# Kernel tuning notes

Hardware: AMD Instinct MI355X
Metric: run time of the kernel (lower is better)

## Reference

```python
import jax, jax.numpy as jnp
import numpy as np

DIM = 512
K_ALL = 11
K_TOP = 4
DOMAIN = 10
EPS = 1e-12
NEG_INF = -1e30

def _normalize(x):
    n = jnp.linalg.norm(x, axis=-1, keepdims=True)
    return x / jnp.maximum(n, EPS)

def _leaky(x):
    return jax.nn.leaky_relu(x, 0.01)

def setup_inputs():
    key = jax.random.key(0)
    ks = jax.random.split(key, 16)
    Bp, Lp, Bg, Lg = 128, 256, 64, 512
    probes = jax.random.normal(ks[0], (1, Bp, Lp, DIM), jnp.float32)
    gallery = jax.random.normal(ks[1], (1, Bg, Lg, DIM), jnp.float32)
    probe_lengths = jax.random.randint(ks[2], (1, Bp), 1, Lp + 1)
    gallery_lengths = jax.random.randint(ks[3], (1, Bg), 1, Lg + 1)
    proxies_p = jax.random.normal(ks[4], (K_ALL, DIM), jnp.float32) * 0.06
    proxies_g = jax.random.normal(ks[5], (K_ALL, DIM), jnp.float32) * 0.06
    transform_W = jax.random.normal(ks[6], (DOMAIN, DIM), jnp.float32) * 0.06
    transform_b = jnp.zeros((DOMAIN,), jnp.float32)
    probe_W = jnp.eye(DIM, dtype=jnp.float32)  # nn.init.eye_
    probe_b = jnp.zeros((DIM,), jnp.float32)
    # pooler MLP weights stacked over the 11 experts; init_weights: N(0, 0.001), zero bias
    pool_W1 = jax.random.normal(ks[7], (K_ALL, 2 * DIM, 3 * DIM), jnp.float32) * 1e-3
    pool_b1 = jnp.zeros((K_ALL, 2 * DIM), jnp.float32)
    pool_W2 = jax.random.normal(ks[8], (K_ALL, 2 * DIM, 2 * DIM), jnp.float32) * 1e-3
    pool_b2 = jnp.zeros((K_ALL, 2 * DIM), jnp.float32)
    pool_W3 = jax.random.normal(ks[9], (K_ALL, DIM, 2 * DIM), jnp.float32) * 1e-3
    pool_b3 = jnp.zeros((K_ALL, DIM), jnp.float32)
    return dict(probes=probes, gallery=gallery, probe_lengths=probe_lengths,
                gallery_lengths=gallery_lengths, proxies_p=proxies_p, proxies_g=proxies_g,
                transform_W=transform_W, transform_b=transform_b, probe_W=probe_W,
                probe_b=probe_b, pool_W1=pool_W1, pool_b1=pool_b1, pool_W2=pool_W2,
                pool_b2=pool_b2, pool_W3=pool_W3, pool_b3=pool_b3)

def reference(probes, gallery, probe_lengths, gallery_lengths, proxies_p, proxies_g,
              transform_W, transform_b, probe_W, probe_b,
              pool_W1, pool_b1, pool_W2, pool_b2, pool_W3, pool_b3):
    def fuse(feat, length, proxies, use_probe_linear):
        # feat: [L, D], length: scalar int; masked equivalent of feat[:length]
        L = feat.shape[0]
        fmask = (jnp.arange(L) < length).astype(feat.dtype)[:, None]  # [L, 1]
        lp = jnp.maximum(length, 1).astype(feat.dtype)
        normed = _normalize(feat)
        tf = _normalize(feat @ transform_W.T + transform_b)        # [L, 10]
        tp = _normalize(proxies @ transform_W.T + transform_b)      # [K_ALL, 10]
        sims = tf @ tp.T                                            # [L, K_ALL]
        gsim = (sims * fmask).sum(0)                                # [K_ALL]
        _, idx = jax.lax.top_k(gsim, K_TOP)
        mean = (feat * fmask).sum(0) / lp                           # [D]
        var = (((feat - mean) ** 2) * fmask).sum(0) / lp            # biased variance
        summary = jnp.concatenate([jnp.tile(mean[None], (K_TOP, 1)),
                                   jnp.tile(var[None], (K_TOP, 1)),
                                   proxies[idx]], axis=-1)          # [K_TOP, 3D]
        # expert-gathered pooler MLPs (dropout = identity in eval)
        h = _leaky(jnp.einsum('koi,ki->ko', pool_W1[idx], summary) + pool_b1[idx])
        h = _leaky(jnp.einsum('koi,ki->ko', pool_W2[idx], h) + pool_b2[idx])
        ctx = _leaky(jnp.einsum('koi,ki->ko', pool_W3[idx], h) + pool_b3[idx])  # [K_TOP, D]
        q = feat @ probe_W.T + probe_b if use_probe_linear else feat
        scores = q @ ctx.T                                          # [L, K_TOP]
        scores = jnp.where(fmask > 0, scores, NEG_INF)
        w = jax.nn.softmax(scores, axis=0)                          # softmax over set dim
        return jnp.einsum('ld,lk->kd', normed, w)                   # [K_TOP, D]

    p, g = probes[0], gallery[0]
    pl, gl = probe_lengths[0], gallery_lengths[0]
    final_probe = jax.vmap(lambda f, l: fuse(f, l, proxies_p, True))(p, pl)
    final_gallery = jax.vmap(lambda f, l: fuse(f, l, proxies_g, False))(g, gl)
    return (final_probe,
            proxies_p @ transform_W.T + transform_b,
            final_gallery,
            proxies_g @ transform_W.T + transform_b)
```

## Files before the change

### kernel.cpp

```cpp
#include <hip/hip_runtime.h>
#include <hip/hip_bf16.h>

namespace {

using us = unsigned short;
typedef __attribute__((ext_vector_type(8))) short bf16x8;
typedef __attribute__((ext_vector_type(4))) float f32x4;
typedef __attribute__((ext_vector_type(4))) unsigned short us4;
typedef __attribute__((ext_vector_type(4))) unsigned int u32x4;

constexpr int DIM_ = 512, KALL = 11, DOM = 10, NPROBE = 128, NSETS = 192;
constexpr int LPR = 256, LGA = 512;

constexpr size_t O_OUT1 = 0;
constexpr size_t O_OUT2 = (size_t)NPROBE * 4 * DIM_;
constexpr size_t O_OUT3 = O_OUT2 + KALL * DOM;
constexpr size_t O_OUT4 = O_OUT3 + (size_t)64 * 4 * DIM_;

constexpr size_t F_TP   = 64;
constexpr size_t F_IDX  = 320;
constexpr size_t F_S0A  = 1600;
constexpr size_t F_WQ   = 4096;
constexpr size_t F_GP   = 495616;
constexpr size_t F_SUMM = 514048;
constexpr size_t F_H1   = 612352;
constexpr size_t F_PART = F_H1;
constexpr size_t F_CTXW = F_H1;
constexpr size_t F_H2   = 1693696;
constexpr size_t F_ACC  = F_H2;
constexpr size_t F_CTX  = 2775040;
constexpr size_t F_WT   = 3315712;
constexpr size_t F_BEFF = 3446784;
constexpr size_t WS_FLOATS = F_BEFF + 2 * KALL * 1024;
constexpr size_t WS_BYTES  = WS_FLOATS * 4;

__device__ __forceinline__ float b2f(us u) { return __uint_as_float(((unsigned)u) << 16); }
__device__ __forceinline__ us f2b(float x) {
    unsigned u = __float_as_uint(x);
    u += 0x7FFF + ((u >> 16) & 1);
    return (us)(u >> 16);
}
__device__ __forceinline__ float ldT(const float* p) { return *p; }
__device__ __forceinline__ float ldT(const us* p) { return b2f(*p); }
__device__ __forceinline__ void stT(float* p, float v) { *p = v; }
__device__ __forceinline__ void stT(us* p, float v) { *p = f2b(v); }

__device__ __forceinline__ bf16x8 loadA(const us* p) { return *(const bf16x8*)p; }
__device__ __forceinline__ bf16x8 loadA(const float* p) {
    f32x4 a = *(const f32x4*)p, b = *(const f32x4*)(p + 4);
    bf16x8 r;
#pragma unroll
    for (int j = 0; j < 4; ++j) { r[j] = (short)f2b(a[j]); r[4 + j] = (short)f2b(b[j]); }
    return r;
}
__device__ __forceinline__ bf16x8 pack8(f32x4 a, f32x4 b) {
    bf16x8 r;
#pragma unroll
    for (int j = 0; j < 4; ++j) { r[j] = (short)f2b(a[j]); r[4 + j] = (short)f2b(b[j]); }
    return r;
}

__device__ __forceinline__ void gload_lds16(const us* g, us* l) {
    __builtin_amdgcn_global_load_lds(
        (const __attribute__((address_space(1))) void*)g,
        (__attribute__((address_space(3))) void*)l, 16, 0, 0);
}

__device__ __forceinline__ void decode64(int bx, int& set, int& base, int& L) {
    if (bx < 512) { set = bx >> 2; base = (bx & 3) * 64; L = LPR; }
    else { set = NPROBE + ((bx - 512) >> 3); base = ((bx - 512) & 7) * 64; L = LGA; }
}

__global__ void detect_kernel(const unsigned int* probeW_bits, int* flag) {
    if (threadIdx.x == 0) *flag = (probeW_bits[0] == 0x3F800000u) ? 0 : 1;
}

template <typename T>
__device__ void proxies_body(const T* pp, const T* pg, const T* tW, const T* tb,
                             float* wsf, T* dout) {
    int b = blockIdx.x;
    int fam = b / KALL, i = b % KALL;
    int lane = threadIdx.x;
    const T* src = fam ? pg : pp;
    float t[DOM];
#pragma unroll
    for (int r = 0; r < DOM; ++r) t[r] = 0.f;
    for (int d = lane; d < DIM_; d += 64) {
        float x = ldT(src + (size_t)i * DIM_ + d);
#pragma unroll
        for (int r = 0; r < DOM; ++r) t[r] += x * ldT(tW + (size_t)r * DIM_ + d);
    }
#pragma unroll
    for (int off = 32; off >= 1; off >>= 1)
#pragma unroll
        for (int r = 0; r < DOM; ++r) t[r] += __shfl_xor(t[r], off, 64);
#pragma unroll
    for (int r = 0; r < DOM; ++r) t[r] += ldT(tb + r);
    float nn = 0.f;
#pragma unroll
    for (int r = 0; r < DOM; ++r) nn += t[r] * t[r];
    float inv = 1.0f / fmaxf(sqrtf(nn), 1e-12f);
    if (lane < DOM) {
        size_t base = fam ? O_OUT4 : O_OUT2;
        stT(dout + base + i * DOM + lane, t[lane]);
        wsf[F_TP + fam * 128 + i * DOM + lane] = t[lane] * inv;
    }
}
__global__ void proxies_kernel(const int* flag, const void* pp, const void* pg,
                               const void* tW, const void* tb, float* wsf, void* dout) {
    if (*flag)
        proxies_body<us>((const us*)pp, (const us*)pg, (const us*)tW, (const us*)tb, wsf, (us*)dout);
    else
        proxies_body<float>((const float*)pp, (const float*)pg, (const float*)tW, (const float*)tb, wsf, (float*)dout);
}

template <typename T>
__device__ void pbias_body(const T* W1, const T* b1, const T* pp, const T* pg, float* beff) {
    int bx = blockIdx.x;
    int e = bx >> 4, ch = bx & 15;
    int tid = threadIdx.x;
    int om = tid >> 2, sub = tid & 3;
    int m = ch * 64 + om;
    const T* wr = W1 + ((size_t)e * 1024 + m) * 1536 + 1024 + sub * 128;
    const T* pr = pp + (size_t)e * DIM_ + sub * 128;
    const T* gr = pg + (size_t)e * DIM_ + sub * 128;
    float sp = 0.f, sg = 0.f;
    if constexpr (sizeof(T) == 2) {
#pragma unroll 4
        for (int k = 0; k < 128; k += 2) {
            unsigned wv = *(const unsigned*)(wr + k);
            unsigned pv = *(const unsigned*)(pr + k);
            unsigned gv = *(const unsigned*)(gr + k);
            float w0 = __uint_as_float(wv << 16), w1 = __uint_as_float(wv & 0xFFFF0000u);
            float p0 = __uint_as_float(pv << 16), p1 = __uint_as_float(pv & 0xFFFF0000u);
            float g0 = __uint_as_float(gv << 16), g1 = __uint_as_float(gv & 0xFFFF0000u);
            sp += w0 * p0 + w1 * p1;
            sg += w0 * g0 + w1 * g1;
        }
    } else {
#pragma unroll 2
        for (int k = 0; k < 128; k += 4) {
            f32x4 wv = *(const f32x4*)(wr + k);
            f32x4 pv = *(const f32x4*)(pr + k);
            f32x4 gv = *(const f32x4*)(gr + k);
#pragma unroll
            for (int q = 0; q < 4; ++q) { sp += wv[q] * pv[q]; sg += wv[q] * gv[q]; }
        }
    }
    sp += __shfl_xor(sp, 1, 64); sp += __shfl_xor(sp, 2, 64);
    sg += __shfl_xor(sg, 1, 64); sg += __shfl_xor(sg, 2, 64);
    if (sub == 0) {
        float bb = ldT(b1 + (size_t)e * 1024 + m);
        beff[(size_t)e * 1024 + m] = bb + sp;
        beff[(size_t)(KALL + e) * 1024 + m] = bb + sg;
    }
}
__global__ void pbias_kernel(const int* flag, const void* W1, const void* b1,
                             const void* pp, const void* pg, float* beff) {
    if (*flag)
        pbias_body<us>((const us*)W1, (const us*)b1, (const us*)pp, (const us*)pg, beff);
    else
        pbias_body<float>((const float*)W1, (const float*)b1, (const float*)pp, (const float*)pg, beff);
}

template <typename T>
__device__ void sims_body(const T* probes, const T* gallery, const int* plen,
                          const int* glen, const T* tW, float* wsf) {
    int bx = blockIdx.x, set, base, L;
    decode64(bx, set, base, L);
    bool probe = set < NPROBE;
    int len = probe ? plen[set] : glen[set - NPROBE];
    int len_eff = min(max(len, 1), L);
    float* GP = wsf + F_GP + (size_t)bx * 12;
    float* PART = wsf + F_PART + (size_t)bx * 1024;
    int tid = threadIdx.x;
    int nvalid = len_eff - base;
    if (nvalid <= 0) {
        if (tid < KALL) GP[tid] = 0.f;
        for (int d = tid; d < 1024; d += 256) PART[d] = 0.f;
        return;
    }
    nvalid = min(nvalid, 64);
    const T* feat = probe ? probes + (size_t)set * L * DIM_
                          : gallery + (size_t)(set - NPROBE) * L * DIM_;
    __shared__ __align__(16) float tile[4][320];
    __shared__ float tpl[KALL * DOM];
    __shared__ float gs[16];
    __shared__ float psum[DIM_], psq[DIM_];
    if (tid < KALL * DOM) tpl[tid] = wsf[F_TP + (probe ? 0 : 128) + tid];
    if (tid < 16) gs[tid] = 0.f;
    psum[tid] = 0.f; psum[tid + 256] = 0.f;
    psq[tid] = 0.f; psq[tid + 256] = 0.f;
    __syncthreads();

    int w = tid >> 6, lane = tid & 63, lm = lane & 15, quad = lane >> 4;

    {
        int cl = lane;
        const T* fb = feat + (size_t)base * DIM_ + cl * 8;
        float asum[8] = {0,0,0,0,0,0,0,0}, asq[8] = {0,0,0,0,0,0,0,0};
        for (int r = w; r < nvalid; r += 8) {
            bool two = (r + 4 < nvalid);
            float f0[8], f1[8];
            if constexpr (sizeof(T) == 2) {
                u32x4 ra = *(const u32x4*)(fb + (size_t)r * DIM_);
                u32x4 rb = two ? *(const u32x4*)(fb + (size_t)(r + 4) * DIM_)
                               : (u32x4){0, 0, 0, 0};
#pragma unroll
                for (int q = 0; q < 4; ++q) {
                    f0[2*q]   = __uint_as_float(ra[q] << 16);
                    f0[2*q+1] = __uint_as_float(ra[q] & 0xFFFF0000u);
                    f1[2*q]   = __uint_as_float(rb[q] << 16);
                    f1[2*q+1] = __uint_as_float(rb[q] & 0xFFFF0000u);
                }
            } else {
                const T* rp = fb + (size_t)r * DIM_;
                f32x4 a0 = *(const f32x4*)rp, a1 = *(const f32x4*)(rp + 4);
#pragma unroll
                for (int j = 0; j < 4; ++j) { f0[j] = a0[j]; f0[4+j] = a1[j]; }
                if (two) {
                    const T* rq = fb + (size_t)(r + 4) * DIM_;
                    f32x4 b0 = *(const f32x4*)rq, b1 = *(const f32x4*)(rq + 4);
#pragma unroll
                    for (int j = 0; j < 4; ++j) { f1[j] = b0[j]; f1[4+j] = b1[j]; }
                } else {
#pragma unroll
                    for (int j = 0; j < 8; ++j) f1[j] = 0.f;
                }
            }
#pragma unroll
            for (int j = 0; j < 8; ++j) {
                asum[j] += f0[j] + f1[j];
                asq[j] += f0[j] * f0[j] + f1[j] * f1[j];
            }
        }
#pragma unroll
        for (int j = 0; j < 8; ++j) {
            atomicAdd(&psum[cl * 8 + j], asum[j]);
            atomicAdd(&psq[cl * 8 + j], asq[j]);
        }
    }
    __syncthreads();
    PART[tid] = psum[tid]; PART[tid + 256] = psum[tid + 256];
    PART[512 + tid] = psq[tid]; PART[768 + tid] = psq[tid + 256];

    bf16x8 bq[16];
#pragma unroll
    for (int s = 0; s < 16; ++s) {
        if (lm < DOM) bq[s] = loadA(tW + (size_t)lm * DIM_ + s * 32 + quad * 8);
        else bq[s] = (bf16x8){0, 0, 0, 0, 0, 0, 0, 0};
    }
    int m0 = base + w * 16;
    const T* Ap = feat + (size_t)(m0 + lm) * DIM_ + quad * 8;
    f32x4 acc = (f32x4){0.f, 0.f, 0.f, 0.f};
    float vsq = 0.f;
#pragma unroll
    for (int s = 0; s < 16; ++s) {
        bf16x8 a;
        if constexpr (sizeof(T) == 2) {
            a = *(const bf16x8*)(Ap + s * 32);
#pragma unroll
            for (int j = 0; j < 8; ++j) { float x = b2f((us)a[j]); vsq += x * x; }
        } else {
            f32x4 p0 = *(const f32x4*)(Ap + s * 32), p1 = *(const f32x4*)(Ap + s * 32 + 4);
#pragma unroll
            for (int j = 0; j < 4; ++j) {
                vsq += p0[j] * p0[j] + p1[j] * p1[j];
                a[j] = (short)f2b(p0[j]); a[4 + j] = (short)f2b(p1[j]);
            }
        }
        acc = __builtin_amdgcn_mfma_f32_16x16x32_bf16(a, bq[s], acc, 0, 0, 0);
    }
    vsq += __shfl_xor(vsq, 16, 64);
    vsq += __shfl_xor(vsq, 32, 64);
    {
        int rown = m0 + lm;
        if (quad == 0 && rown < len_eff)
            wsf[F_WQ + (size_t)set * 2560 + (size_t)rown * 5 + 4] =
                1.0f / fmaxf(sqrtf(vsq), 1e-12f);
    }
#pragma unroll
    for (int r = 0; r < 4; ++r) tile[w][(quad * 4 + r) * 20 + lm] = acc[r];
    __syncthreads();

    float gacc[KALL];
#pragma unroll
    for (int k = 0; k < KALL; ++k) gacc[k] = 0.f;
    if (lane < 16) {
        int row = m0 + lane;
        if (row < len_eff) {
            const float* tr = &tile[w][lane * 20];
            f32x4 t0 = *(const f32x4*)tr, t1 = *(const f32x4*)(tr + 4);
            float tv[DOM] = {t0[0], t0[1], t0[2], t0[3], t1[0], t1[1], t1[2], t1[3], tr[8], tr[9]};
            float nn = 0.f;
#pragma unroll
            for (int r = 0; r < DOM; ++r) nn += tv[r] * tv[r];
            float inv = 1.0f / fmaxf(sqrtf(nn), 1e-12f);
#pragma unroll
            for (int k = 0; k < KALL; ++k) {
                float s = 0.f;
#pragma unroll
                for (int r = 0; r < DOM; ++r) s += tv[r] * tpl[k * DOM + r];
                gacc[k] = s * inv;
            }
        }
    }
#pragma unroll
    for (int off = 8; off >= 1; off >>= 1)
#pragma unroll
        for (int k = 0; k < KALL; ++k) gacc[k] += __shfl_xor(gacc[k], off, 64);
    if (lane == 0)
#pragma unroll
        for (int k = 0; k < KALL; ++k) atomicAdd(&gs[k], gacc[k]);
    __syncthreads();
    if (tid < KALL) GP[tid] = gs[tid];
}
__global__ __launch_bounds__(256, 3) void sims_kernel(const int* flag, const void* probes,
        const void* gallery, const int* plen, const int* glen, const void* tW, float* wsf) {
    if (*flag) sims_body<us>((const us*)probes, (const us*)gallery, plen, glen, (const us*)tW, wsf);
    else sims_body<float>((const float*)probes, (const float*)gallery, plen, glen, (const float*)tW, wsf);
}

__global__ void statsfin_kernel(const int* plen, const int* glen, float* wsf) {
    int set = blockIdx.x, tid = threadIdx.x;
    bool probe = set < NPROBE;
    int len = probe ? plen[set] : glen[set - NPROBE];
    float lp = (float)max(len, 1);
    int nch = probe ? 4 : 8;
    int cb = probe ? set * 4 : 512 + (set - NPROBE) * 8;
    const float* P = wsf + F_PART + (size_t)cb * 1024;
    us* SUMM = (us*)(wsf + F_SUMM);
    for (int d = tid; d < DIM_; d += 256) {
        float s = 0.f, q = 0.f;
        for (int c = 0; c < nch; ++c) {
            s += P[(size_t)c * 1024 + d];
            q += P[(size_t)c * 1024 + 512 + d];
        }
        float m = s / lp;
        float v = q / lp - m * m;
        SUMM[(size_t)set * 1024 + d] = f2b(m);
        SUMM[(size_t)set * 1024 + DIM_ + d] = f2b(v);
    }
    if (tid == 0) {
        int gb = probe ? set * 4 : 512 + (set - NPROBE) * 8;
        float g[KALL];
        for (int i = 0; i < KALL; ++i) {
            float s = 0.f;
            for (int c = 0; c < nch; ++c) s += wsf[F_GP + (size_t)(gb + c) * 12 + i];
            g[i] = s;
        }
        int* idx4 = (int*)(wsf + F_IDX);
        for (int kk = 0; kk < 4; ++kk) {
            int bi = 0; float bv = g[0];
            for (int i = 1; i < KALL; ++i)
                if (g[i] > bv) { bv = g[i]; bi = i; }
            idx4[set * 4 + kk] = bi;
            g[bi] = -3e38f;
        }
    }
}

template <typename T>
__device__ void wt_body(const T* W, us* WT) {
    __shared__ us t[64][65];
    int bi = blockIdx.y * 64, bj = blockIdx.x * 64, tid = threadIdx.x;
    for (int i = tid; i < 4096; i += 256) {
        int r = i >> 6, cc = i & 63;
        t[r][cc] = (sizeof(T) == 2) ? ((const us*)W)[(size_t)(bi + r) * DIM_ + bj + cc]
                                    : f2b(ldT(W + (size_t)(bi + r) * DIM_ + bj + cc));
    }
    __syncthreads();
    for (int i = tid; i < 4096; i += 256) {
        int r = i >> 6, cc = i & 63;
        WT[(size_t)(bj + r) * DIM_ + bi + cc] = t[cc][r];
    }
}
__global__ void wt_kernel(const int* flag, const void* W, us* WT) {
    if (*flag) wt_body<us>((const us*)W, WT);
    else wt_body<float>((const float*)W, WT);
}

template <int M, int KS, int L1>
__global__ __launch_bounds__(256) void mlp_one(const int* flag, const void* Wv,
        const void* biasv, const us* X, us* Y, const float* beff) {
    constexpr int MT = M / 64;
    constexpr int NK = 16;
    int flagv = *flag;
    __shared__ us SM[8192];
    int bx = blockIdx.x;
    int nt = bx / (MT * KALL);
    int rem = bx - nt * (MT * KALL);
    int e = rem % KALL;
    int mt = rem / KALL;
    int tid = threadIdx.x, w = tid >> 6, lane = tid & 63;
    int lm = lane & 15, quad = lane >> 4;
    int s0 = nt * 64;
    const size_t aoff = ((size_t)e * M + mt * 64 + w * 16 + lm) * KS + quad * 8;
    const float* AF = (const float*)Wv + aoff;
    const us*    AB = (const us*)Wv + aoff;
    int xrow0 = (L1 ? 0 : e * NSETS) + s0;
    int slot0 = w * 64 + lane, slot1 = slot0 + 256;
    int brow0 = slot0 >> 3, bcol0 = (slot0 & 7) ^ (brow0 & 7);
    int brow1 = slot1 >> 3, bcol1 = (slot1 & 7) ^ (brow1 & 7);
    const us* Xs0 = X + ((size_t)(xrow0 + brow0)) * 1024 + bcol0 * 8;
    const us* Xs1 = X + ((size_t)(xrow0 + brow1)) * 1024 + bcol1 * 8;
    us* ls0 = SM + slot0 * 8;
    us* ls1 = SM + slot1 * 8;

    f32x4 acc[4];
#pragma unroll
    for (int j = 0; j < 4; ++j) acc[j] = (f32x4){0.f, 0.f, 0.f, 0.f};

    bf16x8 a0[2], a1[2];
    f32x4 pan[4];

    auto issueB = [&](int par, int k0) {
        gload_lds16(Xs0 + k0, ls0 + par * 4096);
        gload_lds16(Xs1 + k0, ls1 + par * 4096);
    };
    auto loadAx = [&](int k0, bf16x8* adst) {
        if (flagv) {
            adst[0] = *(const bf16x8*)(AB + k0);
            adst[1] = *(const bf16x8*)(AB + k0 + 32);
        } else {
            pan[0] = *(const f32x4*)(AF + k0);
            pan[1] = *(const f32x4*)(AF + k0 + 4);
            pan[2] = *(const f32x4*)(AF + k0 + 32);
            pan[3] = *(const f32x4*)(AF + k0 + 36);
        }
    };
    auto packA = [&](bf16x8* adst) {
        if (!flagv) {
            adst[0] = pack8(pan[0], pan[1]);
            adst[1] = pack8(pan[2], pan[3]);
        }
    };
    auto compute = [&](int par, const bf16x8* a) {
        const us* Bb = SM + par * 4096;
#pragma unroll
        for (int ks = 0; ks < 2; ++ks)
#pragma unroll
            for (int j = 0; j < 4; ++j) {
                int br = j * 16 + lm;
                int cg = ks * 4 + quad;
                bf16x8 b = *(const bf16x8*)(Bb + br * 64 + ((cg ^ (br & 7)) * 8));
                acc[j] = __builtin_amdgcn_mfma_f32_16x16x32_bf16(a[ks], b, acc[j], 0, 0, 0);
            }
    };

    issueB(0, 0);
    loadAx(0, a0);
    packA(a0);
    __syncthreads();
#pragma unroll 1
    for (int t = 0; t < NK; t += 2) {
        int k1 = (t + 1) * 64, k2 = (t + 2) * 64;
        if (t + 1 < NK) { issueB(1, k1); loadAx(k1, a1); }
        compute(0, a0);
        if (t + 1 < NK) packA(a1);
        __syncthreads();
        if (t + 1 < NK) {
            if (t + 2 < NK) { issueB(0, k2); loadAx(k2, a0); }
            compute(1, a1);
            if (t + 2 < NK) packA(a0);
            __syncthreads();
        }
    }

    int m0 = mt * 64 + w * 16 + quad * 4;
    float bv[4];
    if (L1) {
        const float* be = beff + ((size_t)((nt < 2) ? 0 : KALL) + e) * 1024 + m0;
#pragma unroll
        for (int r = 0; r < 4; ++r) bv[r] = be[r];
    } else {
#pragma unroll
        for (int r = 0; r < 4; ++r)
            bv[r] = flagv ? b2f(((const us*)biasv)[(size_t)e * M + m0 + r])
                          : ((const float*)biasv)[(size_t)e * M + m0 + r];
    }
#pragma unroll
    for (int j = 0; j < 4; ++j) {
        int s = s0 + j * 16 + lm;
        us4 pk;
#pragma unroll
        for (int r = 0; r < 4; ++r) {
            float v = acc[j][r] + bv[r];
            v = v > 0.f ? v : 0.01f * v;
            pk[r] = f2b(v);
        }
        *(us4*)(Y + ((size_t)e * NSETS + s) * M + m0) = pk;
    }
}

__global__ void fold_kernel(const us* CTX, const us* WT, us* CTXW) {
    int nt = blockIdx.x, mtb = blockIdx.y;
    int e = mtb >> 1, sub = mtb & 1;
    int row0 = e * NSETS + sub * 64;
    int tid = threadIdx.x, w = tid >> 6, lane = tid & 63;
    int lm = lane & 15, quad = lane >> 4, kq = quad * 8;
    const us* Ap = CTX + ((size_t)row0 + w * 16 + lm) * DIM_ + kq;
    int n0 = nt * 64;
    const us* Bp = WT + (size_t)(n0 + lm) * DIM_ + kq;
    f32x4 acc[4];
#pragma unroll
    for (int j = 0; j < 4; ++j) acc[j] = (f32x4){0.f, 0.f, 0.f, 0.f};
#pragma unroll 2
    for (int kc = 0; kc < DIM_; kc += 32) {
        bf16x8 a = *(const bf16x8*)(Ap + kc);
#pragma unroll
        for (int j = 0; j < 4; ++j) {
            bf16x8 b = *(const bf16x8*)(Bp + kc + (size_t)j * 16 * DIM_);
            acc[j] = __builtin_amdgcn_mfma_f32_16x16x32_bf16(a, b, acc[j], 0, 0, 0);
        }
    }
    int mrow = row0 + w * 16 + quad * 4;
#pragma unroll
    for (int j = 0; j < 4; ++j)
#pragma unroll
        for (int r = 0; r < 4; ++r)
            CTXW[(size_t)(mrow + r) * DIM_ + n0 + j * 16 + lm] = f2b(acc[j][r]);
}

template <typename T>
__device__ void s0a_body(const us* CTX, const T* pb, float* S0A) {
    int tid = threadIdx.x, w = tid >> 6, lane = tid & 63;
    int row = blockIdx.x * 4 + w;
    bf16x8 cv = *(const bf16x8*)(CTX + (size_t)row * DIM_ + lane * 8);
    float s = 0.f;
#pragma unroll
    for (int j = 0; j < 8; ++j) s += b2f((us)cv[j]) * ldT(pb + lane * 8 + j);
#pragma unroll
    for (int off = 32; off >= 1; off >>= 1) s += __shfl_xor(s, off, 64);
    if (lane == 0) S0A[row] = s;
}
__global__ void s0a_kernel(const int* flag, const us* CTX, const void* pb, float* S0A) {
    if (*flag) s0a_body<us>(CTX, (const us*)pb, S0A);
    else s0a_body<float>(CTX, (const float*)pb, S0A);
}

template <typename T>
__device__ void score_body(const T* probes, const T* gallery, const int* plen,
                           const int* glen, float* wsf) {
    int bx = blockIdx.x, set, base, L;
    decode64(bx, set, base, L);
    bool probe = set < NPROBE;
    int len = probe ? plen[set] : glen[set - NPROBE];
    int len_eff = min(max(len, 1), L);
    if (base >= len_eff) return;
    const T* feat = probe ? probes + (size_t)set * L * DIM_
                          : gallery + (size_t)(set - NPROBE) * L * DIM_;
    int tid = threadIdx.x, w = tid >> 6, lane = tid & 63;
    int lm = lane & 15, quad = lane >> 4;
    const int* idx4 = (const int*)(wsf + F_IDX);
    const us* CTXW = (const us*)(wsf + F_CTXW);
    const us* CTXR = (const us*)(wsf + F_CTX);
    bf16x8 bq[16];
    float s0v = 0.f;
    if (lm < 4) {
        int row = idx4[set * 4 + lm] * NSETS + set;
        const us* src = (probe ? CTXW : CTXR) + (size_t)row * DIM_ + quad * 8;
#pragma unroll
        for (int s = 0; s < 16; ++s) bq[s] = *(const bf16x8*)(src + s * 32);
        s0v = probe ? wsf[F_S0A + row] : 0.f;
    } else {
#pragma unroll
        for (int s = 0; s < 16; ++s) bq[s] = (bf16x8){0, 0, 0, 0, 0, 0, 0, 0};
    }
    int m0 = base + w * 16;
    const T* Ap = feat + (size_t)(m0 + lm) * DIM_ + quad * 8;
    f32x4 acc = (f32x4){0.f, 0.f, 0.f, 0.f};
#pragma unroll
    for (int s = 0; s < 16; ++s) {
        bf16x8 a = loadA(Ap + s * 32);
        acc = __builtin_amdgcn_mfma_f32_16x16x32_bf16(a, bq[s], acc, 0, 0, 0);
    }
    if (lm < 4) {
        float* wq = wsf + F_WQ + (size_t)set * 2560;
#pragma unroll
        for (int r = 0; r < 4; ++r) {
            int row = m0 + quad * 4 + r;
            wq[(size_t)row * 5 + lm] = acc[r] + s0v;
        }
    }
}
__global__ __launch_bounds__(256, 3) void score_kernel(const int* flag, const void* probes,
        const void* gallery, const int* plen, const int* glen, float* wsf) {
    if (*flag) score_body<us>((const us*)probes, (const us*)gallery, plen, glen, wsf);
    else score_body<float>((const float*)probes, (const float*)gallery, plen, glen, wsf);
}

__global__ void softmax_kernel(const int* plen, const int* glen, float* wsf) {
    int set = blockIdx.x, tid = threadIdx.x, k = tid >> 6, lane = tid & 63;
    bool probe = set < NPROBE;
    int L = probe ? LPR : LGA;
    int len = probe ? plen[set] : glen[set - NPROBE];
    int len_eff = min(max(len, 1), L);
    float* wq = wsf + F_WQ + (size_t)set * 2560;
    float cv[8];
    int n = 0;
    float m = -3e38f;
    for (int l = lane; l < len_eff; l += 64) {
        cv[n] = wq[(size_t)l * 5 + k];
        m = fmaxf(m, cv[n]);
        ++n;
    }
#pragma unroll
    for (int off = 32; off >= 1; off >>= 1) m = fmaxf(m, __shfl_xor(m, off, 64));
    float se = 0.f;
    for (int i = 0; i < n; ++i) se += __expf(cv[i] - m);
#pragma unroll
    for (int off = 32; off >= 1; off >>= 1) se += __shfl_xor(se, off, 64);
    float invs = 1.0f / se;
    n = 0;
    for (int l = lane; l < len_eff; l += 64) {
        wq[(size_t)l * 5 + k] = __expf(cv[n] - m) * invs * wq[(size_t)l * 5 + 4];
        ++n;
    }
}

template <typename T>
__device__ void accum_body(const T* probes, const T* gallery, const int* plen,
                           const int* glen, float* wsf) {
    int bx = blockIdx.x, set = bx >> 2, c = bx & 3;
    bool probe = set < NPROBE;
    int L = probe ? LPR : LGA;
    const T* feat = probe ? probes + (size_t)set * L * DIM_
                          : gallery + (size_t)(set - NPROBE) * L * DIM_;
    int len = probe ? plen[set] : glen[set - NPROBE];
    int len_eff = min(max(len, 1), L);
    int r0 = (c * len_eff) >> 2, r1 = ((c + 1) * len_eff) >> 2;
    int tid = threadIdx.x, g = tid >> 8, t = tid & 255;
    __shared__ float cf[512];
    __shared__ float pbuf[2048];
    int nr = r1 - r0;
    const float* wq = wsf + F_WQ + (size_t)set * 2560;
    for (int p = tid; p < nr * 4; p += 512)
        cf[p] = wq[(size_t)(r0 + (p >> 2)) * 5 + (p & 3)];
    __syncthreads();
    float ac[8] = {0.f, 0.f, 0.f, 0.f, 0.f, 0.f, 0.f, 0.f};
#pragma unroll 4
    for (int l = r0 + g; l < r1; l += 2) {
        float f0, f1;
        if constexpr (sizeof(T) == 2) {
            unsigned u = *(const unsigned*)((const us*)feat + (size_t)l * DIM_ + t * 2);
            f0 = __uint_as_float(u << 16);
            f1 = __uint_as_float(u & 0xFFFF0000u);
        } else {
            const T* rp = feat + (size_t)l * DIM_ + t * 2;
            f0 = rp[0]; f1 = rp[1];
        }
        f32x4 cc = *(const f32x4*)&cf[(l - r0) * 4];
#pragma unroll
        for (int k = 0; k < 4; ++k) {
            ac[k * 2] += f0 * cc[k];
            ac[k * 2 + 1] += f1 * cc[k];
        }
    }
    if (g == 1) {
#pragma unroll
        for (int i = 0; i < 8; ++i) pbuf[i * 256 + t] = ac[i];
    }
    __syncthreads();
    if (g == 0) {
        float* P = wsf + F_ACC + (size_t)bx * 2048;
#pragma unroll
        for (int k = 0; k < 4; ++k) {
            P[k * 512 + t * 2] = ac[k * 2] + pbuf[(k * 2) * 256 + t];
            P[k * 512 + t * 2 + 1] = ac[k * 2 + 1] + pbuf[(k * 2 + 1) * 256 + t];
        }
    }
}
__global__ __launch_bounds__(512) void accum_kernel(const int* flag, const void* probes,
        const void* gallery, const int* plen, const int* glen, float* wsf) {
    if (*flag) accum_body<us>((const us*)probes, (const us*)gallery, plen, glen, wsf);
    else accum_body<float>((const float*)probes, (const float*)gallery, plen, glen, wsf);
}

template <typename T>
__device__ void reduce_body(const float* wsf, T* dout) {
    int set = blockIdx.x, d = threadIdx.x;
    const float* A = wsf + F_ACC + (size_t)set * 4 * 2048;
    size_t ob = (set < NPROBE) ? O_OUT1 + (size_t)set * 2048
                               : O_OUT3 + (size_t)(set - NPROBE) * 2048;
#pragma unroll
    for (int k = 0; k < 4; ++k) {
        float s = A[k * 512 + d] + A[2048 + k * 512 + d] + A[4096 + k * 512 + d] + A[6144 + k * 512 + d];
        stT(dout + ob + k * 512 + d, s);
    }
}
__global__ __launch_bounds__(512) void reduce_kernel(const int* flag, const float* wsf, void* dout) {
    if (*flag) reduce_body<us>(wsf, (us*)dout);
    else reduce_body<float>(wsf, (float*)dout);
}

}

extern "C" void kernel_launch(void* const* d_in, const int* in_sizes, int n_in,
                              void* d_out, int out_size, void* d_ws, size_t ws_size,
                              hipStream_t stream) {
    if (ws_size < WS_BYTES) return;
    float* wsf = (float*)d_ws;
    int* flag = (int*)d_ws;
    us* SUMM = (us*)(wsf + F_SUMM);
    us* H1 = (us*)(wsf + F_H1);
    us* H2 = (us*)(wsf + F_H2);
    us* CTXb = (us*)(wsf + F_CTX);
    us* CTXW = (us*)(wsf + F_CTXW);
    us* WT = (us*)(wsf + F_WT);
    const int* plen = (const int*)d_in[2];
    const int* glen = (const int*)d_in[3];

    detect_kernel<<<1, 64, 0, stream>>>((const unsigned int*)d_in[8], flag);
    proxies_kernel<<<22, 64, 0, stream>>>(flag, d_in[4], d_in[5], d_in[6], d_in[7], wsf, d_out);
    pbias_kernel<<<176, 256, 0, stream>>>(flag, d_in[10], d_in[11], d_in[4], d_in[5], wsf + F_BEFF);
    wt_kernel<<<dim3(8, 8), 256, 0, stream>>>(flag, d_in[8], WT);
    sims_kernel<<<1024, 256, 0, stream>>>(flag, d_in[0], d_in[1], plen, glen, d_in[6], wsf);
    statsfin_kernel<<<NSETS, 256, 0, stream>>>(plen, glen, wsf);

    mlp_one<1024, 1536, 1><<<3 * 16 * KALL, 256, 0, stream>>>(
        flag, d_in[10], nullptr, SUMM, H1, wsf + F_BEFF);
    mlp_one<1024, 1024, 0><<<3 * 16 * KALL, 256, 0, stream>>>(
        flag, d_in[12], d_in[13], H1, H2, nullptr);
    mlp_one<512, 1024, 0><<<3 * 8 * KALL, 256, 0, stream>>>(
        flag, d_in[14], d_in[15], H2, CTXb, nullptr);

    fold_kernel<<<dim3(8, 22), 256, 0, stream>>>(CTXb, WT, CTXW);
    s0a_kernel<<<528, 256, 0, stream>>>(flag, CTXb, d_in[9], wsf + F_S0A);
    score_kernel<<<1024, 256, 0, stream>>>(flag, d_in[0], d_in[1], plen, glen, wsf);
    softmax_kernel<<<NSETS, 256, 0, stream>>>(plen, glen, wsf);
    accum_kernel<<<NSETS * 4, 512, 0, stream>>>(flag, d_in[0], d_in[1], plen, glen, wsf);
    reduce_kernel<<<NSETS, 512, 0, stream>>>(flag, wsf, d_out);
}
```

Measured before the change: 430.5 us.

## Stage feature chunk in swizzled LDS to reuse for stats and MFMA

The stats pass now writes each 64-row feature chunk into a 64KB XOR-swizzled LDS buffer as bf16 while accumulating sums. The MFMA projection then reads A operands from LDS instead of reloading them from global memory, so the second global read of the chunk is removed. The cost is large LDS usage, which lowers occupancy, so the launch-bounds occupancy hint is dropped. The fp32 path's row-norm computation now uses bf16-rounded values.

After: 462.0 us. 7.3% more time.

```diff
diff --git a/kernel.cpp b/kernel.cpp
--- a/kernel.cpp
+++ b/kernel.cpp
@@ -183,6 +183,7 @@
     nvalid = min(nvalid, 64);
     const T* feat = probe ? probes + (size_t)set * L * DIM_
                           : gallery + (size_t)(set - NPROBE) * L * DIM_;
+    __shared__ __align__(16) us FB[64 * 512];
     __shared__ __align__(16) float tile[4][320];
     __shared__ float tpl[KALL * DOM];
     __shared__ float gs[16];
@@ -196,48 +197,41 @@
     int w = tid >> 6, lane = tid & 63, lm = lane & 15, quad = lane >> 4;
 
     {
-        int cl = lane;
-        const T* fb = feat + (size_t)base * DIM_ + cl * 8;
+        const T* fb = feat + (size_t)base * DIM_ + lane * 8;
         float asum[8] = {0,0,0,0,0,0,0,0}, asq[8] = {0,0,0,0,0,0,0,0};
-        for (int r = w; r < nvalid; r += 8) {
-            bool two = (r + 4 < nvalid);
-            float f0[8], f1[8];
-            if constexpr (sizeof(T) == 2) {
-                u32x4 ra = *(const u32x4*)(fb + (size_t)r * DIM_);
-                u32x4 rb = two ? *(const u32x4*)(fb + (size_t)(r + 4) * DIM_)
-                               : (u32x4){0, 0, 0, 0};
-#pragma unroll
-                for (int q = 0; q < 4; ++q) {
-                    f0[2*q]   = __uint_as_float(ra[q] << 16);
-                    f0[2*q+1] = __uint_as_float(ra[q] & 0xFFFF0000u);
-                    f1[2*q]   = __uint_as_float(rb[q] << 16);
-                    f1[2*q+1] = __uint_as_float(rb[q] & 0xFFFF0000u);
+#pragma unroll 4
+        for (int r = w; r < 64; r += 4) {
+            us* dst = FB + r * 512 + ((lane ^ (r & 7)) * 8);
+            if (r < nvalid) {
+                float f[8];
+                if constexpr (sizeof(T) == 2) {
+                    u32x4 ra = *(const u32x4*)(fb + (size_t)r * DIM_);
+                    *(u32x4*)dst = ra;
+#pragma unroll
+                    for (int q = 0; q < 4; ++q) {
+                        f[2*q]   = __uint_as_float(ra[q] << 16);
+                        f[2*q+1] = __uint_as_float(ra[q] & 0xFFFF0000u);
+                    }
+                } else {
+                    f32x4 a0 = *(const f32x4*)(fb + (size_t)r * DIM_);
+                    f32x4 a1 = *(const f32x4*)(fb + (size_t)r * DIM_ + 4);
+#pragma unroll
+                    for (int j = 0; j < 4; ++j) { f[j] = a0[j]; f[4+j] = a1[j]; }
+                    *(bf16x8*)dst = pack8(a0, a1);
+                }
+#pragma unroll
+                for (int j = 0; j < 8; ++j) {
+                    asum[j] += f[j];
+                    asq[j] += f[j] * f[j];
                 }
             } else {
-                const T* rp = fb + (size_t)r * DIM_;
-                f32x4 a0 = *(const f32x4*)rp, a1 = *(const f32x4*)(rp + 4);
-#pragma unroll
-                for (int j = 0; j < 4; ++j) { f0[j] = a0[j]; f0[4+j] = a1[j]; }
-                if (two) {
-                    const T* rq = fb + (size_t)(r + 4) * DIM_;
-                    f32x4 b0 = *(const f32x4*)rq, b1 = *(const f32x4*)(rq + 4);
-#pragma unroll
-                    for (int j = 0; j < 4; ++j) { f1[j] = b0[j]; f1[4+j] = b1[j]; }
-                } else {
-#pragma unroll
-                    for (int j = 0; j < 8; ++j) f1[j] = 0.f;
-                }
+                *(bf16x8*)dst = (bf16x8){0, 0, 0, 0, 0, 0, 0, 0};
             }
-#pragma unroll
-            for (int j = 0; j < 8; ++j) {
-                asum[j] += f0[j] + f1[j];
-                asq[j] += f0[j] * f0[j] + f1[j] * f1[j];
-            }
         }
 #pragma unroll
         for (int j = 0; j < 8; ++j) {
-            atomicAdd(&psum[cl * 8 + j], asum[j]);
-            atomicAdd(&psq[cl * 8 + j], asq[j]);
+            atomicAdd(&psum[lane * 8 + j], asum[j]);
+            atomicAdd(&psq[lane * 8 + j], asq[j]);
         }
     }
     __syncthreads();
@@ -251,24 +245,16 @@
         else bq[s] = (bf16x8){0, 0, 0, 0, 0, 0, 0, 0};
     }
     int m0 = base + w * 16;
-    const T* Ap = feat + (size_t)(m0 + lm) * DIM_ + quad * 8;
+    int arow = w * 16 + lm;
+    const us* Ab = FB + arow * 512;
+    int aswz = arow & 7;
     f32x4 acc = (f32x4){0.f, 0.f, 0.f, 0.f};
     float vsq = 0.f;
 #pragma unroll
     for (int s = 0; s < 16; ++s) {
-        bf16x8 a;
-        if constexpr (sizeof(T) == 2) {
-            a = *(const bf16x8*)(Ap + s * 32);
-#pragma unroll
-            for (int j = 0; j < 8; ++j) { float x = b2f((us)a[j]); vsq += x * x; }
-        } else {
-            f32x4 p0 = *(const f32x4*)(Ap + s * 32), p1 = *(const f32x4*)(Ap + s * 32 + 4);
-#pragma unroll
-            for (int j = 0; j < 4; ++j) {
-                vsq += p0[j] * p0[j] + p1[j] * p1[j];
-                a[j] = (short)f2b(p0[j]); a[4 + j] = (short)f2b(p1[j]);
-            }
-        }
+        bf16x8 a = *(const bf16x8*)(Ab + (((s * 4 + quad) ^ aswz) * 8));
+#pragma unroll
+        for (int j = 0; j < 8; ++j) { float x = b2f((us)a[j]); vsq += x * x; }
         acc = __builtin_amdgcn_mfma_f32_16x16x32_bf16(a, bq[s], acc, 0, 0, 0);
     }
     vsq += __shfl_xor(vsq, 16, 64);
@@ -315,7 +301,7 @@
     __syncthreads();
     if (tid < KALL) GP[tid] = gs[tid];
 }
-__global__ __launch_bounds__(256, 3) void sims_kernel(const int* flag, const void* probes,
+__global__ __launch_bounds__(256) void sims_kernel(const int* flag, const void* probes,
         const void* gallery, const int* plen, const int* glen, const void* tW, float* wsf) {
     if (*flag) sims_body<us>((const us*)probes, (const us*)gallery, plen, glen, (const us*)tW, wsf);
     else sims_body<float>((const float*)probes, (const float*)gallery, plen, glen, (const float*)tW, wsf);
```
